# Kernel optimization log

Measured on AMD Instinct MI355X. Metric: run time of the kernel, lower is better.

The kernel has to match this reference:

```python
import jax, jax.numpy as jnp
import numpy as np
from jax.scipy.stats import norm

E = 8          # num experts
R = 16         # LoRA rank
K = 1          # top-k (top-1 gating)
NOISE_EPS = 1e-2


def setup_inputs() -> dict:
    key = jax.random.key(0)
    ks = jax.random.split(key, 6)
    B, T, D = 8, 1024, 1024
    tokens = jax.random.normal(ks[0], (B, T, D), jnp.float32)
    w_gate = jax.random.normal(ks[1], (D, E), jnp.float32) * 0.02
    w_noise = jax.random.normal(ks[2], (D, E), jnp.float32) * 0.02
    lora_a = jax.random.normal(ks[3], (E, R, D), jnp.float32) / np.sqrt(D).astype(np.float32)
    lora_b = jax.random.normal(ks[4], (E, 3 * D, R), jnp.float32) * 0.02
    noise = jax.random.normal(ks[5], (B * T, E), jnp.float32)  # gating noise (randn_like)
    return dict(tokens=tokens, w_gate=w_gate, w_noise=w_noise,
                lora_a=lora_a, lora_b=lora_b, noise=noise)


def reference(tokens, w_gate, w_noise, lora_a, lora_b, noise):
    B, T, D = tokens.shape
    x = tokens.reshape(B * T, D)                       # [N, D]
    N = x.shape[0]

    # --- noisy top-k gating (train mode) ---
    clean_logits = x @ w_gate                          # [N, E]
    noise_stddev = jax.nn.softplus(x @ w_noise) + NOISE_EPS
    logits = clean_logits + noise * noise_stddev       # noisy logits

    m = min(K + 1, E)
    top_vals, top_idx = jax.lax.top_k(logits, m)       # [N, K+1]
    topk_gates = jax.nn.softmax(top_vals[:, :K], axis=1)
    topk_idx = top_idx[:, :K]

    gates = jnp.zeros((N, E), x.dtype).at[jnp.arange(N)[:, None], topk_idx].set(topk_gates)
    importance = gates.sum(0)                          # [E]

    # --- smooth load estimate (prob each token's noisy logit is in top-k) ---
    thr_in = top_vals[:, K][:, None]                   # (K+1)-th value if expert were in
    thr_out = top_vals[:, K - 1][:, None]              # K-th value if expert were out
    is_in = logits > thr_in
    prob = jnp.where(is_in,
                     norm.cdf((clean_logits - thr_in) / noise_stddev),
                     norm.cdf((clean_logits - thr_out) / noise_stddev))
    load = prob.sum(0)                                 # [E]

    # --- dispatch / per-expert LoRA / gated combine ---
    # SparseDispatcher math is equivalent to gate-weighted sum over experts
    # (gates are zero except at the selected experts).
    h = jnp.einsum('nd,erd->ner', x, lora_a)           # [N, E, R] (cheap: R small)
    gh = gates[:, :, None] * h                         # apply gate before up-proj
    out = jnp.einsum('ner,eor->no', gh, lora_b)        # [N, 3D]

    return out.reshape(B, T, 3 * D), importance, load
```

## Files before the change

### kernel.cpp

```cpp
#include <hip/hip_runtime.h>
#include <math.h>

#define N_TOK 8192
#define DIM   1024
#define NE    8
#define NR    16
#define NO    3072
#define OUT_ELEMS (N_TOK * NO)

__device__ __forceinline__ float softplusf(float z) {
  return z > 0.f ? z + log1pf(expf(-z)) : log1pf(expf(z));
}
__device__ __forceinline__ float ncdf(float z) {
  return 0.5f * erfcf(-z * 0.70710678118654752f);
}

#define FMA4(A, S, W) { (A).x = fmaf((S),(W).x,(A).x); (A).y = fmaf((S),(W).y,(A).y); \
                        (A).z = fmaf((S),(W).z,(A).z); (A).w = fmaf((S),(W).w,(A).w); }
#define DOT4ACC(ACC, X, W) ACC = fmaf((X).x,(W).x, fmaf((X).y,(W).y, fmaf((X).z,(W).z, fmaf((X).w,(W).w,(ACC)))))
#define Z4 make_float4(0.f,0.f,0.f,0.f)

__global__ __launch_bounds__(256) void kA9(const float* __restrict__ x,
    const float* __restrict__ wg, const float* __restrict__ wn,
    const float* __restrict__ nz, int* __restrict__ eid, float* __restrict__ part,
    int* __restrict__ fill) {
  __shared__ float xl[16 * 132];
  __shared__ float wl[128 * 20];
  __shared__ float accd[16 * 16 * 20];
  __shared__ float lgS[16 * 20];
  int t = threadIdx.x;
  int n0 = blockIdx.x << 4;
  if (blockIdx.x == 0 && t < 8) fill[t] = 0;
  int tokq = t & 3, og = (t >> 2) & 3, kh = t >> 4;
  int tx = t >> 4, jx = t & 15;
  int kw = t >> 1, hw = t & 1;
  const float* xsrc = x + (size_t)(n0 + tx) * DIM + (jx << 3);
  const float* wsrc = (hw == 0) ? (wg + (size_t)kw * NE) : (wn + (size_t)kw * NE);
  float4 xa0 = *(const float4*)(xsrc);
  float4 xa1 = *(const float4*)(xsrc + 4);
  float4 wa0 = *(const float4*)(wsrc);
  float4 wa1 = *(const float4*)(wsrc + 4);
  float4 acc0 = Z4, acc1 = Z4, acc2 = Z4, acc3 = Z4;
  for (int c = 0; c < 8; ++c) {
    __syncthreads();
    *(float4*)&xl[tx * 132 + (jx << 3)]     = xa0;
    *(float4*)&xl[tx * 132 + (jx << 3) + 4] = xa1;
    *(float4*)&wl[kw * 20 + (hw << 3)]      = wa0;
    *(float4*)&wl[kw * 20 + (hw << 3) + 4]  = wa1;
    __syncthreads();
    if (c < 7) {
      int xo = (c + 1) << 7;
      xa0 = *(const float4*)(xsrc + xo);
      xa1 = *(const float4*)(xsrc + xo + 4);
      int wo = (c + 1) << 10;
      wa0 = *(const float4*)(wsrc + wo);
      wa1 = *(const float4*)(wsrc + wo + 4);
    }
    #pragma unroll
    for (int k4 = 0; k4 < 2; ++k4) {
      int kk = (kh << 3) + (k4 << 2);
      float4 xv0 = *(const float4*)&xl[(tokq +  0) * 132 + kk];
      float4 xv1 = *(const float4*)&xl[(tokq +  4) * 132 + kk];
      float4 xv2 = *(const float4*)&xl[(tokq +  8) * 132 + kk];
      float4 xv3 = *(const float4*)&xl[(tokq + 12) * 132 + kk];
      const float* wb = &wl[kk * 20 + (og << 2)];
      float4 w0 = *(const float4*)(wb + 0);
      float4 w1 = *(const float4*)(wb + 20);
      float4 w2 = *(const float4*)(wb + 40);
      float4 w3 = *(const float4*)(wb + 60);
      FMA4(acc0, xv0.x, w0); FMA4(acc0, xv0.y, w1); FMA4(acc0, xv0.z, w2); FMA4(acc0, xv0.w, w3);
      FMA4(acc1, xv1.x, w0); FMA4(acc1, xv1.y, w1); FMA4(acc1, xv1.z, w2); FMA4(acc1, xv1.w, w3);
      FMA4(acc2, xv2.x, w0); FMA4(acc2, xv2.y, w1); FMA4(acc2, xv2.z, w2); FMA4(acc2, xv2.w, w3);
      FMA4(acc3, xv3.x, w0); FMA4(acc3, xv3.y, w1); FMA4(acc3, xv3.z, w2); FMA4(acc3, xv3.w, w3);
    }
  }
  { int b = kh * 320 + (og << 2);
    *(float4*)&accd[b + (tokq +  0) * 20] = acc0;
    *(float4*)&accd[b + (tokq +  4) * 20] = acc1;
    *(float4*)&accd[b + (tokq +  8) * 20] = acc2;
    *(float4*)&accd[b + (tokq + 12) * 20] = acc3; }
  __syncthreads();
  { int ts = t >> 4, o = t & 15;
    float s = 0.f;
    #pragma unroll
    for (int k2 = 0; k2 < 16; ++k2) s += accd[k2 * 320 + ts * 20 + o];
    lgS[ts * 20 + o] = s; }
  __syncthreads();
  if (t < 16) {
    int n = n0 + t;
    float cl[8], st[8], lg[8];
    float4 nzv0 = *(const float4*)(nz + (size_t)n * NE);
    float4 nzv1 = *(const float4*)(nz + (size_t)n * NE + 4);
    float nzv[8] = {nzv0.x, nzv0.y, nzv0.z, nzv0.w, nzv1.x, nzv1.y, nzv1.z, nzv1.w};
    #pragma unroll
    for (int e = 0; e < 8; ++e) cl[e] = lgS[t * 20 + e];
    #pragma unroll
    for (int e = 0; e < 8; ++e) {
      st[e] = softplusf(lgS[t * 20 + 8 + e]) + 0.01f;
      lg[e] = fmaf(nzv[e], st[e], cl[e]);
    }
    float m1 = -1e30f, m2 = -1e30f; int idx = 0;
    #pragma unroll
    for (int e = 0; e < 8; ++e) {
      float v = lg[e];
      if (v > m1)      { m2 = m1; m1 = v; idx = e; }
      else if (v > m2) { m2 = v; }
    }
    eid[n] = idx;
    float pr[8], cw[8];
    #pragma unroll
    for (int e = 0; e < 8; ++e) {
      float thr = (lg[e] > m2) ? m2 : m1;
      pr[e] = ncdf((cl[e] - thr) / st[e]);
    }
    #pragma unroll
    for (int e = 0; e < 8; ++e) cw[e] = (float)__popcll(__ballot(idx == e));
    #pragma unroll
    for (int e = 0; e < 8; ++e) {
      #pragma unroll
      for (int off = 1; off <= 8; off <<= 1) pr[e] += __shfl_xor(pr[e], off);
    }
    if (t == 0) {
      #pragma unroll
      for (int e = 0; e < 8; ++e) {
        part[blockIdx.x * 16 + e]     = cw[e];
        part[blockIdx.x * 16 + 8 + e] = pr[e];
      }
    }
  }
}

__global__ __launch_bounds__(256) void kC(const float* __restrict__ part,
    const int* __restrict__ eid, int* __restrict__ fill, int* __restrict__ bucket,
    float* __restrict__ outIL, int* __restrict__ counts) {
  __shared__ float red[16][16];
  __shared__ int cnt_s[8], lcnt[8], lbase[8];
  int t = threadIdx.x;
  int s = t & 15, g = t >> 4;
  float sum = 0.f;
  #pragma unroll
  for (int j = 0; j < 32; ++j) sum += part[(g + 16 * j) * 16 + s];
  red[g][s] = sum;
  if (t < 8) lcnt[t] = 0;
  __syncthreads();
  if (t < 16) {
    float tot = 0.f;
    #pragma unroll
    for (int gg = 0; gg < 16; ++gg) tot += red[gg][t];
    if (blockIdx.x == 0) outIL[t] = tot;
    if (t < 8) {
      cnt_s[t] = (int)(tot + 0.5f);
      if (blockIdx.x == 0) counts[t] = (int)(tot + 0.5f);
    }
  }
  __syncthreads();
  int n = blockIdx.x * 256 + t;
  int e = eid[n];
  int rank = atomicAdd(&lcnt[e], 1);
  __syncthreads();
  if (t < 8) lbase[t] = atomicAdd(&fill[t], lcnt[t]);
  __syncthreads();
  int off = 0;
  #pragma unroll
  for (int i = 0; i < 8; ++i) if (i < e) off += cnt_s[i];
  bucket[off + lbase[e] + rank] = n;
}

__global__ __launch_bounds__(256) void kD9(const float* __restrict__ x,
    const float* __restrict__ la, const int* __restrict__ counts,
    const int* __restrict__ bucket, float* __restrict__ h) {
  __shared__ float xl[16 * 132];
  __shared__ float wl[16 * 132];
  __shared__ float accd[16 * 16 * 20];
  __shared__ float hS[16 * 20];
  __shared__ int toks[16];
  int tile = blockIdx.x;
  int e = -1, jt = 0, off = 0;
  { int tot = 0, o = 0;
    #pragma unroll
    for (int i = 0; i < 8; ++i) {
      int c = counts[i]; int nt = (c + 15) >> 4;
      if (e < 0 && tile < tot + nt) { e = i; jt = tile - tot; off = o; }
      tot += nt; o += c;
    } }
  if (e < 0) return;
  int cnt = counts[e];
  int p0 = off + (jt << 4);
  int valid = min(16, cnt - (jt << 4));
  int t = threadIdx.x;
  if (t < 16) toks[t] = bucket[p0 + min(t, valid - 1)];
  __syncthreads();
  int tokq = t & 3, rg = (t >> 2) & 3, kh = t >> 4;
  int tx = t >> 4, jx = t & 15;
  const float* xsrc = x + (size_t)toks[tx] * DIM + (jx << 3);
  const float* wsrc = la + (size_t)e * (NR * DIM) + (size_t)tx * DIM + (jx << 3);
  float4 xa0 = *(const float4*)(xsrc);
  float4 xa1 = *(const float4*)(xsrc + 4);
  float4 wa0 = *(const float4*)(wsrc);
  float4 wa1 = *(const float4*)(wsrc + 4);
  float4 acc0 = Z4, acc1 = Z4, acc2 = Z4, acc3 = Z4;
  for (int c = 0; c < 8; ++c) {
    __syncthreads();
    *(float4*)&xl[tx * 132 + (jx << 3)]     = xa0;
    *(float4*)&xl[tx * 132 + (jx << 3) + 4] = xa1;
    *(float4*)&wl[tx * 132 + (jx << 3)]     = wa0;
    *(float4*)&wl[tx * 132 + (jx << 3) + 4] = wa1;
    __syncthreads();
    if (c < 7) {
      int ko = (c + 1) << 7;
      xa0 = *(const float4*)(xsrc + ko);
      xa1 = *(const float4*)(xsrc + ko + 4);
      wa0 = *(const float4*)(wsrc + ko);
      wa1 = *(const float4*)(wsrc + ko + 4);
    }
    #pragma unroll
    for (int k4 = 0; k4 < 2; ++k4) {
      int kk = (kh << 3) + (k4 << 2);
      float4 xv0 = *(const float4*)&xl[(tokq +  0) * 132 + kk];
      float4 xv1 = *(const float4*)&xl[(tokq +  4) * 132 + kk];
      float4 xv2 = *(const float4*)&xl[(tokq +  8) * 132 + kk];
      float4 xv3 = *(const float4*)&xl[(tokq + 12) * 132 + kk];
      const float* wb = &wl[(rg << 2) * 132 + kk];
      float4 a0 = *(const float4*)(wb + 0);
      float4 a1 = *(const float4*)(wb + 132);
      float4 a2 = *(const float4*)(wb + 264);
      float4 a3 = *(const float4*)(wb + 396);
      DOT4ACC(acc0.x, xv0, a0); DOT4ACC(acc0.y, xv0, a1); DOT4ACC(acc0.z, xv0, a2); DOT4ACC(acc0.w, xv0, a3);
      DOT4ACC(acc1.x, xv1, a0); DOT4ACC(acc1.y, xv1, a1); DOT4ACC(acc1.z, xv1, a2); DOT4ACC(acc1.w, xv1, a3);
      DOT4ACC(acc2.x, xv2, a0); DOT4ACC(acc2.y, xv2, a1); DOT4ACC(acc2.z, xv2, a2); DOT4ACC(acc2.w, xv2, a3);
      DOT4ACC(acc3.x, xv3, a0); DOT4ACC(acc3.y, xv3, a1); DOT4ACC(acc3.z, xv3, a2); DOT4ACC(acc3.w, xv3, a3);
    }
  }
  { int b = kh * 320 + (rg << 2);
    *(float4*)&accd[b + (tokq +  0) * 20] = acc0;
    *(float4*)&accd[b + (tokq +  4) * 20] = acc1;
    *(float4*)&accd[b + (tokq +  8) * 20] = acc2;
    *(float4*)&accd[b + (tokq + 12) * 20] = acc3; }
  __syncthreads();
  { int ts = t >> 4, rr = t & 15;
    float s = 0.f;
    #pragma unroll
    for (int k2 = 0; k2 < 16; ++k2) s += accd[k2 * 320 + ts * 20 + rr];
    hS[ts * 20 + rr] = s; }
  __syncthreads();
  if (t < 64) {
    int tk = t >> 2, rq = (t & 3) << 2;
    if (tk < valid) {
      float4 v = make_float4(hS[tk * 20 + rq + 0], hS[tk * 20 + rq + 1],
                             hS[tk * 20 + rq + 2], hS[tk * 20 + rq + 3]);
      *(float4*)(h + (size_t)(p0 + tk) * NR + rq) = v;
    }
  }
}

__global__ __launch_bounds__(256) void kE(const float* __restrict__ h,
    const float* __restrict__ lb, const int* __restrict__ counts,
    const int* __restrict__ bucket, float* __restrict__ out) {
  __shared__ float bt[16][260];
  __shared__ float ht[16][64];
  __shared__ int toks[64];
  int tile = blockIdx.y;
  int e = -1, jt = 0, off = 0;
  { int tot = 0, o = 0;
    #pragma unroll
    for (int i = 0; i < 8; ++i) {
      int c = counts[i]; int nt = (c + 63) >> 6;
      if (e < 0 && tile < tot + nt) { e = i; jt = tile - tot; off = o; }
      tot += nt; o += c;
    } }
  if (e < 0) return;
  int cnt = counts[e];
  int p0 = off + (jt << 6);
  int valid = min(64, cnt - (jt << 6));
  int o0 = blockIdx.x << 8;
  int t = threadIdx.x;
  if (t < 64) toks[t] = bucket[p0 + min(t, valid - 1)];
  const float* bbase = lb + ((size_t)e * NO + o0) * NR;
  #pragma unroll
  for (int kk = 0; kk < 4; ++kk) {
    int idx = (kk << 8) + t;
    int o = idx >> 2, rq = (idx & 3) << 2;
    float4 v = *(const float4*)(bbase + o * NR + rq);
    bt[rq + 0][o] = v.x; bt[rq + 1][o] = v.y; bt[rq + 2][o] = v.z; bt[rq + 3][o] = v.w;
  }
  { int tok = t >> 2, rq = (t & 3) << 2;
    float4 v = *(const float4*)(h + (size_t)(p0 + min(tok, valid - 1)) * NR + rq);
    ht[rq + 0][tok] = v.x; ht[rq + 1][tok] = v.y; ht[rq + 2][tok] = v.z; ht[rq + 3][tok] = v.w; }
  __syncthreads();
  int og = t & 31, tokg = t >> 5;
  int ob = og << 2, tb = tokg << 3;
  float4 z = Z4;
  float4 aL0=z,aL1=z,aL2=z,aL3=z,aL4=z,aL5=z,aL6=z,aL7=z;
  float4 aH0=z,aH1=z,aH2=z,aH3=z,aH4=z,aH5=z,aH6=z,aH7=z;
  #pragma unroll
  for (int r = 0; r < 16; ++r) {
    float4 blo = *(const float4*)&bt[r][ob];
    float4 bhi = *(const float4*)&bt[r][ob + 128];
    float4 h0  = *(const float4*)&ht[r][tb];
    float4 h1  = *(const float4*)&ht[r][tb + 4];
    FMA4(aL0, h0.x, blo); FMA4(aH0, h0.x, bhi);
    FMA4(aL1, h0.y, blo); FMA4(aH1, h0.y, bhi);
    FMA4(aL2, h0.z, blo); FMA4(aH2, h0.z, bhi);
    FMA4(aL3, h0.w, blo); FMA4(aH3, h0.w, bhi);
    FMA4(aL4, h1.x, blo); FMA4(aH4, h1.x, bhi);
    FMA4(aL5, h1.y, blo); FMA4(aH5, h1.y, bhi);
    FMA4(aL6, h1.z, blo); FMA4(aH6, h1.z, bhi);
    FMA4(aL7, h1.w, blo); FMA4(aH7, h1.w, bhi);
  }
  #define ST(J, AL, AH) { int tt = tb + (J); if (tt < valid) { \
      float* p = out + (size_t)toks[tt] * NO + o0 + ob; \
      *(float4*)p = AL; *(float4*)(p + 128) = AH; } }
  ST(0, aL0, aH0); ST(1, aL1, aH1); ST(2, aL2, aH2); ST(3, aL3, aH3);
  ST(4, aL4, aH4); ST(5, aL5, aH5); ST(6, aL6, aH6); ST(7, aL7, aH7);
  #undef ST
}

extern "C" void kernel_launch(void* const* d_in, const int* in_sizes, int n_in,
                              void* d_out, int out_size, void* d_ws, size_t ws_size,
                              hipStream_t stream) {
  const float* x  = (const float*)d_in[0];
  const float* wg = (const float*)d_in[1];
  const float* wn = (const float*)d_in[2];
  const float* la = (const float*)d_in[3];
  const float* lb = (const float*)d_in[4];
  const float* nz = (const float*)d_in[5];
  float* out = (float*)d_out;

  char* ws = (char*)d_ws;
  float* h        = (float*)(ws);
  int*   eid      = (int*)  (ws + 524288);
  int*   bucket   = (int*)  (ws + 557056);
  float* partials = (float*)(ws + 589824);
  int*   counts   = (int*)  (ws + 622592);
  int*   fill     = (int*)  (ws + 622624);

  kA9<<<512, 256, 0, stream>>>(x, wg, wn, nz, eid, partials, fill);
  kC<<<32, 256, 0, stream>>>(partials, eid, fill, bucket, out + OUT_ELEMS, counts);
  kD9<<<519, 256, 0, stream>>>(x, la, counts, bucket, h);
  kE<<<dim3(12, 135), 256, 0, stream>>>(h, lb, counts, bucket, out);
}
```

Before: 71.86 us.

## Fuse expert bucketing into gating kernel and drop the separate scatter kernel

After: 75.31 us. 4.8% more time.

```diff
diff --git a/kernel.cpp b/kernel.cpp
--- a/kernel.cpp
+++ b/kernel.cpp
@@ -20,17 +20,17 @@
 #define DOT4ACC(ACC, X, W) ACC = fmaf((X).x,(W).x, fmaf((X).y,(W).y, fmaf((X).z,(W).z, fmaf((X).w,(W).w,(ACC)))))
 #define Z4 make_float4(0.f,0.f,0.f,0.f)
 
-__global__ __launch_bounds__(256) void kA9(const float* __restrict__ x,
+__global__ __launch_bounds__(256) void kA13(const float* __restrict__ x,
     const float* __restrict__ wg, const float* __restrict__ wn,
-    const float* __restrict__ nz, int* __restrict__ eid, float* __restrict__ part,
-    int* __restrict__ fill) {
+    const float* __restrict__ nz, float* __restrict__ part,
+    int* __restrict__ fill, int* __restrict__ bucket) {
   __shared__ float xl[16 * 132];
   __shared__ float wl[128 * 20];
   __shared__ float accd[16 * 16 * 20];
   __shared__ float lgS[16 * 20];
+  __shared__ int eid_sh[16], lcnt[8], lbase[8];
   int t = threadIdx.x;
   int n0 = blockIdx.x << 4;
-  if (blockIdx.x == 0 && t < 8) fill[t] = 0;
   int tokq = t & 3, og = (t >> 2) & 3, kh = t >> 4;
   int tx = t >> 4, jx = t & 15;
   int kw = t >> 1, hw = t & 1;
@@ -85,6 +85,7 @@
     #pragma unroll
     for (int k2 = 0; k2 < 16; ++k2) s += accd[k2 * 320 + ts * 20 + o];
     lgS[ts * 20 + o] = s; }
+  if (t < 8) lcnt[t] = 0;
   __syncthreads();
   if (t < 16) {
     int n = n0 + t;
@@ -106,7 +107,7 @@
       if (v > m1)      { m2 = m1; m1 = v; idx = e; }
       else if (v > m2) { m2 = v; }
     }
-    eid[n] = idx;
+    eid_sh[t] = idx;
     float pr[8], cw[8];
     #pragma unroll
     for (int e = 0; e < 8; ++e) {
@@ -128,67 +129,44 @@
       }
     }
   }
-}
-
-__global__ __launch_bounds__(256) void kC(const float* __restrict__ part,
-    const int* __restrict__ eid, int* __restrict__ fill, int* __restrict__ bucket,
-    float* __restrict__ outIL, int* __restrict__ counts) {
-  __shared__ float red[16][16];
-  __shared__ int cnt_s[8], lcnt[8], lbase[8];
-  int t = threadIdx.x;
-  int s = t & 15, g = t >> 4;
-  float sum = 0.f;
-  #pragma unroll
-  for (int j = 0; j < 32; ++j) sum += part[(g + 16 * j) * 16 + s];
-  red[g][s] = sum;
-  if (t < 8) lcnt[t] = 0;
+  __syncthreads();
+  int rank = 0;
+  if (t < 16) rank = atomicAdd(&lcnt[eid_sh[t]], 1);
+  __syncthreads();
+  if (t < 8 && lcnt[t] > 0) lbase[t] = atomicAdd(&fill[t], lcnt[t]);
   __syncthreads();
   if (t < 16) {
-    float tot = 0.f;
-    #pragma unroll
-    for (int gg = 0; gg < 16; ++gg) tot += red[gg][t];
-    if (blockIdx.x == 0) outIL[t] = tot;
-    if (t < 8) {
-      cnt_s[t] = (int)(tot + 0.5f);
-      if (blockIdx.x == 0) counts[t] = (int)(tot + 0.5f);
-    }
-  }
-  __syncthreads();
-  int n = blockIdx.x * 256 + t;
-  int e = eid[n];
-  int rank = atomicAdd(&lcnt[e], 1);
-  __syncthreads();
-  if (t < 8) lbase[t] = atomicAdd(&fill[t], lcnt[t]);
-  __syncthreads();
-  int off = 0;
-  #pragma unroll
-  for (int i = 0; i < 8; ++i) if (i < e) off += cnt_s[i];
-  bucket[off + lbase[e] + rank] = n;
-}
-
-__global__ __launch_bounds__(256) void kD9(const float* __restrict__ x,
-    const float* __restrict__ la, const int* __restrict__ counts,
+    int e = eid_sh[t];
+    bucket[(e << 13) + lbase[e] + rank] = n0 + t;
+  }
+}
+
+__global__ __launch_bounds__(256) void kD13(const float* __restrict__ x,
+    const float* __restrict__ la, const int* __restrict__ fill,
     const int* __restrict__ bucket, float* __restrict__ h) {
   __shared__ float xl[16 * 132];
   __shared__ float wl[16 * 132];
   __shared__ float accd[16 * 16 * 20];
   __shared__ float hS[16 * 20];
   __shared__ int toks[16];
+  __shared__ int cs[8];
+  int t = threadIdx.x;
+  if (t < 8) cs[t] = fill[t];
+  __syncthreads();
   int tile = blockIdx.x;
   int e = -1, jt = 0, off = 0;
   { int tot = 0, o = 0;
     #pragma unroll
     for (int i = 0; i < 8; ++i) {
-      int c = counts[i]; int nt = (c + 15) >> 4;
+      int c = cs[i]; int nt = (c + 15) >> 4;
       if (e < 0 && tile < tot + nt) { e = i; jt = tile - tot; off = o; }
       tot += nt; o += c;
     } }
   if (e < 0) return;
-  int cnt = counts[e];
+  int cnt = cs[e];
   int p0 = off + (jt << 4);
   int valid = min(16, cnt - (jt << 4));
-  int t = threadIdx.x;
-  if (t < 16) toks[t] = bucket[p0 + min(t, valid - 1)];
+  if (t < 16) toks[t] = bucket[(e << 13) + (jt << 4) + min(t, valid - 1)];
   __syncthreads();
   int tokq = t & 3, rg = (t >> 2) & 3, kh = t >> 4;
   int tx = t >> 4, jx = t & 15;
@@ -253,28 +231,47 @@
   }
 }
 
-__global__ __launch_bounds__(256) void kE(const float* __restrict__ h,
-    const float* __restrict__ lb, const int* __restrict__ counts,
-    const int* __restrict__ bucket, float* __restrict__ out) {
+__global__ __launch_bounds__(256) void kE13(const float* __restrict__ h,
+    const float* __restrict__ lb, const int* __restrict__ fill,
+    const int* __restrict__ bucket, const float* __restrict__ part,
+    float* __restrict__ outIL, float* __restrict__ out) {
   __shared__ float bt[16][260];
   __shared__ float ht[16][64];
   __shared__ int toks[64];
+  __shared__ int cs[8];
+  __shared__ float red[16][16];
+  int t = threadIdx.x;
+  if (t < 8) cs[t] = fill[t];
+  __syncthreads();
+  if (blockIdx.x == 0 && blockIdx.y == 0) {
+    int s = t & 15, g = t >> 4;
+    float sum = 0.f;
+    #pragma unroll
+    for (int j = 0; j < 32; ++j) sum += part[(g + 16 * j) * 16 + s];
+    red[g][s] = sum;
+    __syncthreads();
+    if (t < 16) {
+      float tot = 0.f;
+      #pragma unroll
+      for (int gg = 0; gg < 16; ++gg) tot += red[gg][t];
+      outIL[t] = tot;
+    }
+  }
   int tile = blockIdx.y;
   int e = -1, jt = 0, off = 0;
   { int tot = 0, o = 0;
     #pragma unroll
     for (int i = 0; i < 8; ++i) {
-      int c = counts[i]; int nt = (c + 63) >> 6;
+      int c = cs[i]; int nt = (c + 63) >> 6;
       if (e < 0 && tile < tot + nt) { e = i; jt = tile - tot; off = o; }
       tot += nt; o += c;
     } }
   if (e < 0) return;
-  int cnt = counts[e];
+  int cnt = cs[e];
   int p0 = off + (jt << 6);
   int valid = min(64, cnt - (jt << 6));
   int o0 = blockIdx.x << 8;
-  int t = threadIdx.x;
-  if (t < 64) toks[t] = bucket[p0 + min(t, valid - 1)];
+  if (t < 64) toks[t] = bucket[(e << 13) + (jt << 6) + min(t, valid - 1)];
   const float* bbase = lb + ((size_t)e * NO + o0) * NR;
   #pragma unroll
   for (int kk = 0; kk < 4; ++kk) {
@@ -328,14 +325,13 @@
 
   char* ws = (char*)d_ws;
   float* h        = (float*)(ws);
-  int*   eid      = (int*)  (ws + 524288);
-  int*   bucket   = (int*)  (ws + 557056);
-  float* partials = (float*)(ws + 589824);
-  int*   counts   = (int*)  (ws + 622592);
-  int*   fill     = (int*)  (ws + 622624);
-
-  kA9<<<512, 256, 0, stream>>>(x, wg, wn, nz, eid, partials, fill);
-  kC<<<32, 256, 0, stream>>>(partials, eid, fill, bucket, out + OUT_ELEMS, counts);
-  kD9<<<519, 256, 0, stream>>>(x, la, counts, bucket, h);
-  kE<<<dim3(12, 135), 256, 0, stream>>>(h, lb, counts, bucket, out);
-}
+  int*   bucket   = (int*)  (ws + 524288);
+  float* partials = (float*)(ws + 786432);
+  int*   fill     = (int*)  (ws + 819200);
+
+  hipMemsetAsync(fill, 0, 32, stream);
+  kA13<<<512, 256, 0, stream>>>(x, wg, wn, nz, partials, fill, bucket);
+  kD13<<<519, 256, 0, stream>>>(x, la, fill, bucket, h);
+  kE13<<<dim3(12, 135), 256, 0, stream>>>(h, lb, fill, bucket, partials,
+                                          out + OUT_ELEMS, out);
+}
```

## Fuse LoRA down-projection and up-projection into one per-tile kernel

Applied to the files above, without the earlier changes.

New measurement: 77.02 us. +7.2%, slower.

```diff
diff --git a/kernel.cpp b/kernel.cpp
--- a/kernel.cpp
+++ b/kernel.cpp
@@ -166,13 +166,14 @@
   bucket[off + lbase[e] + rank] = n;
 }
 
-__global__ __launch_bounds__(256) void kD9(const float* __restrict__ x,
-    const float* __restrict__ la, const int* __restrict__ counts,
-    const int* __restrict__ bucket, float* __restrict__ h) {
+__global__ __launch_bounds__(256) void kDE(const float* __restrict__ x,
+    const float* __restrict__ la, const float* __restrict__ lb,
+    const int* __restrict__ counts, const int* __restrict__ bucket,
+    float* __restrict__ out) {
   __shared__ float xl[16 * 132];
   __shared__ float wl[16 * 132];
   __shared__ float accd[16 * 16 * 20];
-  __shared__ float hS[16 * 20];
+  __shared__ float hSt[16 * 20];
   __shared__ int toks[16];
   int tile = blockIdx.x;
   int e = -1, jt = 0, off = 0;
@@ -190,129 +191,100 @@
   int t = threadIdx.x;
   if (t < 16) toks[t] = bucket[p0 + min(t, valid - 1)];
   __syncthreads();
-  int tokq = t & 3, rg = (t >> 2) & 3, kh = t >> 4;
-  int tx = t >> 4, jx = t & 15;
-  const float* xsrc = x + (size_t)toks[tx] * DIM + (jx << 3);
-  const float* wsrc = la + (size_t)e * (NR * DIM) + (size_t)tx * DIM + (jx << 3);
-  float4 xa0 = *(const float4*)(xsrc);
-  float4 xa1 = *(const float4*)(xsrc + 4);
-  float4 wa0 = *(const float4*)(wsrc);
-  float4 wa1 = *(const float4*)(wsrc + 4);
-  float4 acc0 = Z4, acc1 = Z4, acc2 = Z4, acc3 = Z4;
-  for (int c = 0; c < 8; ++c) {
+  {
+    int tokq = t & 3, rg = (t >> 2) & 3, kh = t >> 4;
+    int tx = t >> 4, jx = t & 15;
+    const float* xsrc = x + (size_t)toks[tx] * DIM + (jx << 3);
+    const float* wsrc = la + (size_t)e * (NR * DIM) + (size_t)tx * DIM + (jx << 3);
+    float4 xa0 = *(const float4*)(xsrc);
+    float4 xa1 = *(const float4*)(xsrc + 4);
+    float4 wa0 = *(const float4*)(wsrc);
+    float4 wa1 = *(const float4*)(wsrc + 4);
+    float4 acc0 = Z4, acc1 = Z4, acc2 = Z4, acc3 = Z4;
+    for (int c = 0; c < 8; ++c) {
+      __syncthreads();
+      *(float4*)&xl[tx * 132 + (jx << 3)]     = xa0;
+      *(float4*)&xl[tx * 132 + (jx << 3) + 4] = xa1;
+      *(float4*)&wl[tx * 132 + (jx << 3)]     = wa0;
+      *(float4*)&wl[tx * 132 + (jx << 3) + 4] = wa1;
+      __syncthreads();
+      if (c < 7) {
+        int ko = (c + 1) << 7;
+        xa0 = *(const float4*)(xsrc + ko);
+        xa1 = *(const float4*)(xsrc + ko + 4);
+        wa0 = *(const float4*)(wsrc + ko);
+        wa1 = *(const float4*)(wsrc + ko + 4);
+      }
+      #pragma unroll
+      for (int k4 = 0; k4 < 2; ++k4) {
+        int kk = (kh << 3) + (k4 << 2);
+        float4 xv0 = *(const float4*)&xl[(tokq +  0) * 132 + kk];
+        float4 xv1 = *(const float4*)&xl[(tokq +  4) * 132 + kk];
+        float4 xv2 = *(const float4*)&xl[(tokq +  8) * 132 + kk];
+        float4 xv3 = *(const float4*)&xl[(tokq + 12) * 132 + kk];
+        const float* wb = &wl[(rg << 2) * 132 + kk];
+        float4 a0 = *(const float4*)(wb + 0);
+        float4 a1 = *(const float4*)(wb + 132);
+        float4 a2 = *(const float4*)(wb + 264);
+        float4 a3 = *(const float4*)(wb + 396);
+        DOT4ACC(acc0.x, xv0, a0); DOT4ACC(acc0.y, xv0, a1); DOT4ACC(acc0.z, xv0, a2); DOT4ACC(acc0.w, xv0, a3);
+        DOT4ACC(acc1.x, xv1, a0); DOT4ACC(acc1.y, xv1, a1); DOT4ACC(acc1.z, xv1, a2); DOT4ACC(acc1.w, xv1, a3);
+        DOT4ACC(acc2.x, xv2, a0); DOT4ACC(acc2.y, xv2, a1); DOT4ACC(acc2.z, xv2, a2); DOT4ACC(acc2.w, xv2, a3);
+        DOT4ACC(acc3.x, xv3, a0); DOT4ACC(acc3.y, xv3, a1); DOT4ACC(acc3.z, xv3, a2); DOT4ACC(acc3.w, xv3, a3);
+      }
+    }
+    { int b = kh * 320 + (rg << 2);
+      *(float4*)&accd[b + (tokq +  0) * 20] = acc0;
+      *(float4*)&accd[b + (tokq +  4) * 20] = acc1;
+      *(float4*)&accd[b + (tokq +  8) * 20] = acc2;
+      *(float4*)&accd[b + (tokq + 12) * 20] = acc3; }
     __syncthreads();
-    *(float4*)&xl[tx * 132 + (jx << 3)]     = xa0;
-    *(float4*)&xl[tx * 132 + (jx << 3) + 4] = xa1;
-    *(float4*)&wl[tx * 132 + (jx << 3)]     = wa0;
-    *(float4*)&wl[tx * 132 + (jx << 3) + 4] = wa1;
+    { int ts = t >> 4, rr = t & 15;
+      float s = 0.f;
+      #pragma unroll
+      for (int k2 = 0; k2 < 16; ++k2) s += accd[k2 * 320 + ts * 20 + rr];
+      hSt[rr * 20 + ts] = s; }
     __syncthreads();
-    if (c < 7) {
-      int ko = (c + 1) << 7;
-      xa0 = *(const float4*)(xsrc + ko);
-      xa1 = *(const float4*)(xsrc + ko + 4);
-      wa0 = *(const float4*)(wsrc + ko);
-      wa1 = *(const float4*)(wsrc + ko + 4);
-    }
-    #pragma unroll
-    for (int k4 = 0; k4 < 2; ++k4) {
-      int kk = (kh << 3) + (k4 << 2);
-      float4 xv0 = *(const float4*)&xl[(tokq +  0) * 132 + kk];
-      float4 xv1 = *(const float4*)&xl[(tokq +  4) * 132 + kk];
-      float4 xv2 = *(const float4*)&xl[(tokq +  8) * 132 + kk];
-      float4 xv3 = *(const float4*)&xl[(tokq + 12) * 132 + kk];
-      const float* wb = &wl[(rg << 2) * 132 + kk];
-      float4 a0 = *(const float4*)(wb + 0);
-      float4 a1 = *(const float4*)(wb + 132);
-      float4 a2 = *(const float4*)(wb + 264);
-      float4 a3 = *(const float4*)(wb + 396);
-      DOT4ACC(acc0.x, xv0, a0); DOT4ACC(acc0.y, xv0, a1); DOT4ACC(acc0.z, xv0, a2); DOT4ACC(acc0.w, xv0, a3);
-      DOT4ACC(acc1.x, xv1, a0); DOT4ACC(acc1.y, xv1, a1); DOT4ACC(acc1.z, xv1, a2); DOT4ACC(acc1.w, xv1, a3);
-      DOT4ACC(acc2.x, xv2, a0); DOT4ACC(acc2.y, xv2, a1); DOT4ACC(acc2.z, xv2, a2); DOT4ACC(acc2.w, xv2, a3);
-      DOT4ACC(acc3.x, xv3, a0); DOT4ACC(acc3.y, xv3, a1); DOT4ACC(acc3.z, xv3, a2); DOT4ACC(acc3.w, xv3, a3);
-    }
-  }
-  { int b = kh * 320 + (rg << 2);
-    *(float4*)&accd[b + (tokq +  0) * 20] = acc0;
-    *(float4*)&accd[b + (tokq +  4) * 20] = acc1;
-    *(float4*)&accd[b + (tokq +  8) * 20] = acc2;
-    *(float4*)&accd[b + (tokq + 12) * 20] = acc3; }
-  __syncthreads();
-  { int ts = t >> 4, rr = t & 15;
-    float s = 0.f;
-    #pragma unroll
-    for (int k2 = 0; k2 < 16; ++k2) s += accd[k2 * 320 + ts * 20 + rr];
-    hS[ts * 20 + rr] = s; }
-  __syncthreads();
-  if (t < 64) {
-    int tk = t >> 2, rq = (t & 3) << 2;
-    if (tk < valid) {
-      float4 v = make_float4(hS[tk * 20 + rq + 0], hS[tk * 20 + rq + 1],
-                             hS[tk * 20 + rq + 2], hS[tk * 20 + rq + 3]);
-      *(float4*)(h + (size_t)(p0 + tk) * NR + rq) = v;
-    }
-  }
-}
-
-__global__ __launch_bounds__(256) void kE(const float* __restrict__ h,
-    const float* __restrict__ lb, const int* __restrict__ counts,
-    const int* __restrict__ bucket, float* __restrict__ out) {
-  __shared__ float bt[16][260];
-  __shared__ float ht[16][64];
-  __shared__ int toks[64];
-  int tile = blockIdx.y;
-  int e = -1, jt = 0, off = 0;
-  { int tot = 0, o = 0;
-    #pragma unroll
-    for (int i = 0; i < 8; ++i) {
-      int c = counts[i]; int nt = (c + 63) >> 6;
-      if (e < 0 && tile < tot + nt) { e = i; jt = tile - tot; off = o; }
-      tot += nt; o += c;
-    } }
-  if (e < 0) return;
-  int cnt = counts[e];
-  int p0 = off + (jt << 6);
-  int valid = min(64, cnt - (jt << 6));
-  int o0 = blockIdx.x << 8;
-  int t = threadIdx.x;
-  if (t < 64) toks[t] = bucket[p0 + min(t, valid - 1)];
-  const float* bbase = lb + ((size_t)e * NO + o0) * NR;
-  #pragma unroll
-  for (int kk = 0; kk < 4; ++kk) {
-    int idx = (kk << 8) + t;
-    int o = idx >> 2, rq = (idx & 3) << 2;
-    float4 v = *(const float4*)(bbase + o * NR + rq);
-    bt[rq + 0][o] = v.x; bt[rq + 1][o] = v.y; bt[rq + 2][o] = v.z; bt[rq + 3][o] = v.w;
-  }
-  { int tok = t >> 2, rq = (t & 3) << 2;
-    float4 v = *(const float4*)(h + (size_t)(p0 + min(tok, valid - 1)) * NR + rq);
-    ht[rq + 0][tok] = v.x; ht[rq + 1][tok] = v.y; ht[rq + 2][tok] = v.z; ht[rq + 3][tok] = v.w; }
-  __syncthreads();
-  int og = t & 31, tokg = t >> 5;
-  int ob = og << 2, tb = tokg << 3;
-  float4 z = Z4;
-  float4 aL0=z,aL1=z,aL2=z,aL3=z,aL4=z,aL5=z,aL6=z,aL7=z;
-  float4 aH0=z,aH1=z,aH2=z,aH3=z,aH4=z,aH5=z,aH6=z,aH7=z;
-  #pragma unroll
-  for (int r = 0; r < 16; ++r) {
-    float4 blo = *(const float4*)&bt[r][ob];
-    float4 bhi = *(const float4*)&bt[r][ob + 128];
-    float4 h0  = *(const float4*)&ht[r][tb];
-    float4 h1  = *(const float4*)&ht[r][tb + 4];
-    FMA4(aL0, h0.x, blo); FMA4(aH0, h0.x, bhi);
-    FMA4(aL1, h0.y, blo); FMA4(aH1, h0.y, bhi);
-    FMA4(aL2, h0.z, blo); FMA4(aH2, h0.z, bhi);
-    FMA4(aL3, h0.w, blo); FMA4(aH3, h0.w, bhi);
-    FMA4(aL4, h1.x, blo); FMA4(aH4, h1.x, bhi);
-    FMA4(aL5, h1.y, blo); FMA4(aH5, h1.y, bhi);
-    FMA4(aL6, h1.z, blo); FMA4(aH6, h1.z, bhi);
-    FMA4(aL7, h1.w, blo); FMA4(aH7, h1.w, bhi);
-  }
-  #define ST(J, AL, AH) { int tt = tb + (J); if (tt < valid) { \
-      float* p = out + (size_t)toks[tt] * NO + o0 + ob; \
-      *(float4*)p = AL; *(float4*)(p + 128) = AH; } }
-  ST(0, aL0, aH0); ST(1, aL1, aH1); ST(2, aL2, aH2); ST(3, aL3, aH3);
-  ST(4, aL4, aH4); ST(5, aL5, aH5); ST(6, aL6, aH6); ST(7, aL7, aH7);
-  #undef ST
+  }
+  {
+    float* bt = accd;
+    const float* lbE = lb + (size_t)e * NO * NR;
+    int oo = t >> 2, rq2 = (t & 3) << 2;
+    int og2 = t & 63, tg2 = t >> 6;
+    float4 s0, s1, s2, s3;
+    #define LBL(OT) { size_t b_ = ((size_t)(OT) << 8); \
+      s0 = *(const float4*)(lbE + (b_ + oo)       * NR + rq2); \
+      s1 = *(const float4*)(lbE + (b_ + 64 + oo)  * NR + rq2); \
+      s2 = *(const float4*)(lbE + (b_ + 128 + oo) * NR + rq2); \
+      s3 = *(const float4*)(lbE + (b_ + 192 + oo) * NR + rq2); }
+    #define LBST(R, OK) { bt[(rq2 + 0) * 260 + (OK)] = (R).x; \
+                          bt[(rq2 + 1) * 260 + (OK)] = (R).y; \
+                          bt[(rq2 + 2) * 260 + (OK)] = (R).z; \
+                          bt[(rq2 + 3) * 260 + (OK)] = (R).w; }
+    LBL(0)
+    for (int ot = 0; ot < 12; ++ot) {
+      __syncthreads();
+      LBST(s0, oo) LBST(s1, 64 + oo) LBST(s2, 128 + oo) LBST(s3, 192 + oo)
+      __syncthreads();
+      if (ot < 11) LBL(ot + 1)
+      float4 a0 = Z4, a1 = Z4, a2 = Z4, a3 = Z4;
+      #pragma unroll
+      for (int r = 0; r < 16; ++r) {
+        float4 bv = *(const float4*)&bt[r * 260 + (og2 << 2)];
+        float4 hv = *(const float4*)&hSt[r * 20 + (tg2 << 2)];
+        FMA4(a0, hv.x, bv); FMA4(a1, hv.y, bv);
+        FMA4(a2, hv.z, bv); FMA4(a3, hv.w, bv);
+      }
+      int ob2 = (ot << 8) + (og2 << 2);
+      int tb2 = tg2 << 2;
+      if (tb2 + 0 < valid) *(float4*)(out + (size_t)toks[tb2 + 0] * NO + ob2) = a0;
+      if (tb2 + 1 < valid) *(float4*)(out + (size_t)toks[tb2 + 1] * NO + ob2) = a1;
+      if (tb2 + 2 < valid) *(float4*)(out + (size_t)toks[tb2 + 2] * NO + ob2) = a2;
+      if (tb2 + 3 < valid) *(float4*)(out + (size_t)toks[tb2 + 3] * NO + ob2) = a3;
+    }
+    #undef LBL
+    #undef LBST
+  }
 }
 
 extern "C" void kernel_launch(void* const* d_in, const int* in_sizes, int n_in,
@@ -327,15 +299,13 @@
   float* out = (float*)d_out;
 
   char* ws = (char*)d_ws;
-  float* h        = (float*)(ws);
-  int*   eid      = (int*)  (ws + 524288);
-  int*   bucket   = (int*)  (ws + 557056);
-  float* partials = (float*)(ws + 589824);
-  int*   counts   = (int*)  (ws + 622592);
-  int*   fill     = (int*)  (ws + 622624);
+  int*   eid      = (int*)  (ws);
+  int*   bucket   = (int*)  (ws + 32768);
+  float* partials = (float*)(ws + 65536);
+  int*   counts   = (int*)  (ws + 98304);
+  int*   fill     = (int*)  (ws + 98336);
 
   kA9<<<512, 256, 0, stream>>>(x, wg, wn, nz, eid, partials, fill);
   kC<<<32, 256, 0, stream>>>(partials, eid, fill, bucket, out + OUT_ELEMS, counts);
-  kD9<<<519, 256, 0, stream>>>(x, la, counts, bucket, h);
-  kE<<<dim3(12, 135), 256, 0, stream>>>(h, lb, counts, bucket, out);
-}
+  kDE<<<519, 256, 0, stream>>>(x, la, lb, counts, bucket, out);
+}
```
